# Optimization experiments

Hardware: AMD Instinct MI355X
Metric: run time of the kernel (lower is better)

Reference implementation:

```python
import jax, jax.numpy as jnp
import numpy as np

N = 10000
E = 320000
F_IN = 256
HID = 64
HEADS = 8
NUM_CLASSES = 2
NEG_SLOPE = 0.2


def _glorot(key, shape):
    fan_in, fan_out = shape[0], shape[-1]
    lim = (6.0 / (fan_in + fan_out)) ** 0.5
    return jax.random.uniform(key, shape, jnp.float32, -lim, lim)


def setup_inputs() -> dict:
    key = jax.random.key(0)
    ks = jax.random.split(key, 20)
    x = jax.random.normal(ks[0], (N, F_IN), jnp.float32)
    edge_index = jax.random.randint(ks[1], (2, E), 0, N, jnp.int64)
    d = {
        "x": x,
        "edge_index": edge_index,
        # layer 1: in=256 -> heads=8, C=64, concat -> 512
        "W1": _glorot(ks[2], (F_IN, HEADS * HID)),
        "a_src1": _glorot(ks[3], (HEADS, HID)),
        "a_dst1": _glorot(ks[4], (HEADS, HID)),
        "b1": jnp.zeros((HEADS * HID,), jnp.float32),
        # layer 2: in=512 -> heads=8, C=64, concat -> 512
        "W2": _glorot(ks[5], (HEADS * HID, HEADS * HID)),
        "a_src2": _glorot(ks[6], (HEADS, HID)),
        "a_dst2": _glorot(ks[7], (HEADS, HID)),
        "b2": jnp.zeros((HEADS * HID,), jnp.float32),
        # output conv: in=512 -> heads=1, C=64, no concat
        "W3": _glorot(ks[8], (HEADS * HID, HID)),
        "a_src3": _glorot(ks[9], (1, HID)),
        "a_dst3": _glorot(ks[10], (1, HID)),
        "b3": jnp.zeros((HID,), jnp.float32),
        # classifier
        "lin_W": _glorot(ks[11], (HID, NUM_CLASSES)),
        "lin_b": jnp.zeros((NUM_CLASSES,), jnp.float32),
    }
    return d


def _gat_layer(x, src, dst, W, a_src, a_dst, b, heads, ch, concat):
    # project: [N, H, C]
    h = (x @ W).reshape(-1, heads, ch)
    alpha_src = jnp.sum(h * a_src, axis=-1)  # [N, H]
    alpha_dst = jnp.sum(h * a_dst, axis=-1)  # [N, H]
    # per-edge attention logits (edge j -> i uses src alpha of j, dst alpha of i)
    e = jax.nn.leaky_relu(alpha_src[src] + alpha_dst[dst], NEG_SLOPE)  # [E, H]
    # segment softmax over incoming edges of each destination node
    m = jax.ops.segment_max(e, dst, num_segments=N)  # [N, H]
    m = jnp.where(jnp.isfinite(m), m, 0.0)
    ex = jnp.exp(e - m[dst])
    denom = jax.ops.segment_sum(ex, dst, num_segments=N)
    alpha = ex / (denom[dst] + 1e-16)  # [E, H]
    # weighted message aggregation
    out = jax.ops.segment_sum(h[src] * alpha[:, :, None], dst, num_segments=N)  # [N, H, C]
    if concat:
        out = out.reshape(N, heads * ch)
    else:
        out = out.mean(axis=1)
    return out + b


def reference(x, edge_index, W1, a_src1, a_dst1, b1, W2, a_src2, a_dst2, b2,
              W3, a_src3, a_dst3, b3, lin_W, lin_b):
    # PyG GATConv adds self loops by default
    loop = jnp.arange(N, dtype=edge_index.dtype)
    src = jnp.concatenate([edge_index[0], loop])
    dst = jnp.concatenate([edge_index[1], loop])

    h = _gat_layer(x, src, dst, W1, a_src1, a_dst1, b1, HEADS, HID, True)
    h = jax.nn.elu(h)
    h = _gat_layer(h, src, dst, W2, a_src2, a_dst2, b2, HEADS, HID, True)
    h = jax.nn.elu(h)
    h = _gat_layer(h, src, dst, W3, a_src3, a_dst3, b3, 1, HID, False)
    logits = h @ lin_W + lin_b
    return jax.nn.log_softmax(logits, axis=1)
```

## Files before the change

### kernel.cpp

```cpp
#include <hip/hip_runtime.h>
#include <cmath>

#define NEG 0.2f

typedef __bf16 bf16x8 __attribute__((ext_vector_type(8)));
typedef float  f32x4  __attribute__((ext_vector_type(4)));

__device__ __forceinline__ void async16(const __bf16* g, __bf16* l) {
  __builtin_amdgcn_global_load_lds(
      (const __attribute__((address_space(1))) void*)g,
      (__attribute__((address_space(3))) void*)l, 16, 0, 0);
}
__device__ __forceinline__ f32x4 mfma16(bf16x8 a, bf16x8 b, f32x4 c) {
  return __builtin_amdgcn_mfma_f32_16x16x32_bf16(a, b, c, 0, 0, 0);
}

__global__ void count_kernel(const int* __restrict__ ei, int* __restrict__ counts, int E, int Nn) {
  int e = blockIdx.x * blockDim.x + threadIdx.x;
  if (e >= E + Nn) return;
  int d = (e < E) ? ei[E + e] : (e - E);
  atomicAdd(&counts[d], 1);
}

__global__ __launch_bounds__(1024) void scan_kernel(const int* __restrict__ counts,
                                                    int* __restrict__ row_ptr,
                                                    int* __restrict__ cursor,
                                                    int n, int total) {
  __shared__ int sums[1024];
  int t = threadIdx.x;
  int per = (n + 1023) >> 10;
  int base = t * per;
  int s = 0;
  for (int i = 0; i < per; ++i) { int idx = base + i; if (idx < n) s += counts[idx]; }
  sums[t] = s;
  __syncthreads();
  for (int st = 1; st < 1024; st <<= 1) {
    int v = (t >= st) ? sums[t - st] : 0;
    __syncthreads();
    sums[t] += v;
    __syncthreads();
  }
  int off = (t == 0) ? 0 : sums[t - 1];
  for (int i = 0; i < per; ++i) {
    int idx = base + i;
    if (idx < n) { row_ptr[idx] = off; cursor[idx] = off; off += counts[idx]; }
  }
  if (t == 0) row_ptr[n] = total;
}

__global__ void scatter_kernel(const int* __restrict__ ei, int* __restrict__ cursor,
                               int* __restrict__ src_sorted, int E, int Nn) {
  int e = blockIdx.x * blockDim.x + threadIdx.x;
  if (e >= E + Nn) return;
  int s, d;
  if (e < E) { s = ei[e]; d = ei[E + e]; } else { s = e - E; d = e - E; }
  int pos = atomicAdd(&cursor[d], 1);
  src_sorted[pos] = s;
}

__global__ void prep_kernel(const float* __restrict__ x, __bf16* __restrict__ xsh,
                            __bf16* __restrict__ xsl,
                            const float* __restrict__ W1, __bf16* __restrict__ W1th,
                            const float* __restrict__ W2, __bf16* __restrict__ W2th,
                            const float* __restrict__ W3, __bf16* __restrict__ W3th,
                            int* __restrict__ counts, int Nn) {
  int i = blockIdx.x * blockDim.x + threadIdx.x;
  if (i < Nn) { counts[i] = 0; return; }
  i -= Nn;
  int nx = Nn * 256;
  if (i < nx) {
    float v = x[i];
    __bf16 h = (__bf16)v;
    xsh[i] = h;
    xsl[i] = (__bf16)(v - (float)h);
    return;
  }
  i -= nx;
  if (i < 256 * 512) {
    int k = i / 512, c = i % 512;
    W1th[(size_t)c * 256 + k] = (__bf16)W1[i];
    return;
  }
  i -= 256 * 512;
  if (i < 512 * 512) {
    int k = i / 512, c = i % 512;
    W2th[(size_t)c * 512 + k] = (__bf16)W2[i];
    return;
  }
  i -= 512 * 512;
  if (i < 512 * 64) {
    int k = i / 64, c = i % 64;
    W3th[(size_t)c * 512 + k] = (__bf16)W3[i];
    return;
  }
}

template <bool ASPLIT>
__global__ __launch_bounds__(256, 4) void gemm_v3(
    const __bf16* __restrict__ Ah, const __bf16* __restrict__ Al,
    const __bf16* __restrict__ Bth,
    __bf16* __restrict__ Cb,
    const float* __restrict__ asrc, const float* __restrict__ adst,
    float* __restrict__ als, float* __restrict__ ald,
    int M, int K, int Nc, int PX) {
  __shared__ __bf16 sAh[64 * 64], sBh[128 * 64];
  __shared__ __bf16 sAl[ASPLIT ? 64 * 64 : 64];

  int p = blockIdx.x;
  int c = p & 7, j = p >> 3;
  int x = c * PX + (j >> 2);
  int y = j & 3;
  int rowBase = x * 64, colBase = y * 128;
  if (rowBase >= M) return;

  int tid = threadIdx.x;
  int lane = tid & 63, wave = tid >> 6;
  int r16 = lane & 15, koct = lane >> 4, msk = r16 & 7;

  int fa0 = tid, fa1 = 256 + tid;
  int ar0 = fa0 >> 3, ar1 = fa1 >> 3;
  int as0 = (fa0 & 7) ^ (ar0 & 7);
  int as1 = (fa1 & 7) ^ (ar1 & 7);
  size_t aoff0 = (size_t)min(rowBase + ar0, M - 1) * K + as0 * 8;
  size_t aoff1 = (size_t)min(rowBase + ar1, M - 1) * K + as1 * 8;
  size_t boff[4];
#pragma unroll
  for (int r = 0; r < 4; ++r) {
    int f = r * 256 + tid;
    int col = f >> 3;
    int s = (f & 7) ^ (col & 7);
    boff[r] = (size_t)(colBase + col) * K + s * 8;
  }
  int lb0 = (wave * 64) * 8;
  int lb1 = ((256 + wave * 64)) * 8;
  int lb2 = ((512 + wave * 64)) * 8;
  int lb3 = ((768 + wave * 64)) * 8;

  int arow = wave * 16 + r16;
  f32x4 acc[8] = {};

  for (int k0 = 0; k0 < K; k0 += 64) {
    __syncthreads();
    async16(Ah + aoff0 + k0, sAh + lb0);
    async16(Ah + aoff1 + k0, sAh + lb1);
    if (ASPLIT) {
      async16(Al + aoff0 + k0, sAl + lb0);
      async16(Al + aoff1 + k0, sAl + lb1);
    }
    async16(Bth + boff[0] + k0, sBh + lb0);
    async16(Bth + boff[1] + k0, sBh + lb1);
    async16(Bth + boff[2] + k0, sBh + lb2);
    async16(Bth + boff[3] + k0, sBh + lb3);
    __syncthreads();

#pragma unroll
    for (int kk = 0; kk < 2; ++kk) {
      int ks = ((kk * 4 + koct) ^ msk) * 8;
      bf16x8 ah = *reinterpret_cast<const bf16x8*>(sAh + arow * 64 + ks);
      bf16x8 al;
      if (ASPLIT) al = *reinterpret_cast<const bf16x8*>(sAl + arow * 64 + ks);
      bf16x8 bh[8];
#pragma unroll
      for (int fn = 0; fn < 8; ++fn)
        bh[fn] = *reinterpret_cast<const bf16x8*>(sBh + (fn * 16 + r16) * 64 + ks);
#pragma unroll
      for (int fn = 0; fn < 8; ++fn) {
        acc[fn] = mfma16(ah, bh[fn], acc[fn]);
        if (ASPLIT) acc[fn] = mfma16(al, bh[fn], acc[fn]);
      }
    }
  }

  float asv[8], adv[8];
#pragma unroll
  for (int fn = 0; fn < 8; ++fn) {
    int ai = (y * 2 + (fn >> 2)) * 64 + (fn & 3) * 16 + r16;
    asv[fn] = asrc[ai];
    adv[fn] = adst[ai];
  }
#pragma unroll
  for (int r = 0; r < 4; ++r) {
    int row = rowBase + wave * 16 + koct * 4 + r;
    float psA = 0.f, pdA = 0.f, psB = 0.f, pdB = 0.f;
#pragma unroll
    for (int fn = 0; fn < 8; ++fn) {
      float v = acc[fn][r];
      if (row < M) Cb[(size_t)row * Nc + colBase + fn * 16 + r16] = (__bf16)v;
      if (fn < 4) { psA = fmaf(v, asv[fn], psA); pdA = fmaf(v, adv[fn], pdA); }
      else        { psB = fmaf(v, asv[fn], psB); pdB = fmaf(v, adv[fn], pdB); }
    }
#pragma unroll
    for (int sft = 1; sft < 16; sft <<= 1) {
      psA += __shfl_xor(psA, sft); pdA += __shfl_xor(pdA, sft);
      psB += __shfl_xor(psB, sft); pdB += __shfl_xor(pdB, sft);
    }
    if (r16 == 0 && row < M) {
      als[(size_t)row * 8 + y * 2 + 0] = psA;
      ald[(size_t)row * 8 + y * 2 + 0] = pdA;
      als[(size_t)row * 8 + y * 2 + 1] = psB;
      ald[(size_t)row * 8 + y * 2 + 1] = pdB;
    }
  }
}

__global__ __launch_bounds__(256, 4) void gemm_v2(
    const __bf16* __restrict__ Ah,
    const __bf16* __restrict__ Bth,
    float* __restrict__ Cf,
    const float* __restrict__ asrc, const float* __restrict__ adst,
    float* __restrict__ als, float* __restrict__ ald,
    int M, int K, int Nc) {
  __shared__ __bf16 sAh[128 * 64], sBh[64 * 64];

  int x = blockIdx.x;
  int rowBase = x * 128, colBase = 0;
  if (rowBase >= M) return;

  int tid = threadIdx.x;
  int lane = tid & 63, wave = tid >> 6;
  int r16 = lane & 15, koct = lane >> 4, msk = r16 & 7;

  f32x4 acc[2][4] = {};

  for (int k0 = 0; k0 < K; k0 += 64) {
    __syncthreads();
#pragma unroll
    for (int r = 0; r < 4; ++r) {
      int flat = r * 256 + tid;
      int row = flat >> 3;
      int grow = rowBase + row;
      if (grow >= M) grow = M - 1;
      int s = (flat & 7) ^ (row & 7);
      size_t go = (size_t)grow * K + k0 + s * 8;
      int lb = (r * 256 + wave * 64) * 8;
      async16(Ah + go, sAh + lb);
    }
#pragma unroll
    for (int r = 0; r < 2; ++r) {
      int flat = r * 256 + tid;
      int col = flat >> 3;
      int s = (flat & 7) ^ (col & 7);
      size_t go = (size_t)(colBase + col) * K + k0 + s * 8;
      int lb = (r * 256 + wave * 64) * 8;
      async16(Bth + go, sBh + lb);
    }
    __syncthreads();

#pragma unroll
    for (int kk = 0; kk < 2; ++kk) {
      bf16x8 ah[2], bh[4];
#pragma unroll
      for (int fm = 0; fm < 2; ++fm) {
        int off = (wave * 32 + fm * 16 + r16) * 64 + (((kk * 4 + koct) ^ msk) * 8);
        ah[fm] = *reinterpret_cast<const bf16x8*>(sAh + off);
      }
#pragma unroll
      for (int fn = 0; fn < 4; ++fn) {
        int off = (fn * 16 + r16) * 64 + (((kk * 4 + koct) ^ msk) * 8);
        bh[fn] = *reinterpret_cast<const bf16x8*>(sBh + off);
      }
#pragma unroll
      for (int fm = 0; fm < 2; ++fm)
#pragma unroll
        for (int fn = 0; fn < 4; ++fn)
          acc[fm][fn] = mfma16(ah[fm], bh[fn], acc[fm][fn]);
    }
  }

  float asv[4], adv[4];
#pragma unroll
  for (int fn = 0; fn < 4; ++fn) {
    asv[fn] = asrc[fn * 16 + r16];
    adv[fn] = adst[fn * 16 + r16];
  }
#pragma unroll
  for (int fm = 0; fm < 2; ++fm)
#pragma unroll
    for (int r = 0; r < 4; ++r) {
      int row = rowBase + wave * 32 + fm * 16 + koct * 4 + r;
      float ps = 0.f, pd = 0.f;
#pragma unroll
      for (int fn = 0; fn < 4; ++fn) {
        float v = acc[fm][fn][r];
        ps = fmaf(v, asv[fn], ps);
        pd = fmaf(v, adv[fn], pd);
        if (row < M) Cf[(size_t)row * Nc + fn * 16 + r16] = v;
      }
#pragma unroll
      for (int sft = 1; sft < 16; sft <<= 1) {
        ps += __shfl_xor(ps, sft);
        pd += __shfl_xor(pd, sft);
      }
      if (r16 == 0 && row < M) {
        als[row] = ps;
        ald[row] = pd;
      }
    }
}

__global__ __launch_bounds__(256) void agg8v4_kernel(const __bf16* __restrict__ Hb,
                                                     const float* __restrict__ als,
                                                     const float* __restrict__ ald,
                                                     const float* __restrict__ bias,
                                                     const int* __restrict__ row_ptr,
                                                     const int* __restrict__ src_sorted,
                                                     __bf16* __restrict__ Oh,
                                                     int Nn) {
  int c8 = blockIdx.x & 7;
  int sl = c8 >> 1;
  int chunk = (blockIdx.x >> 3) * 2 + (c8 & 1);
  int lane = threadIdx.x & 63, wave = threadIdx.x >> 6;
  int sub = lane >> 4;
  int cg = lane & 15;
  int n = chunk * 16 + wave * 4 + sub;
  bool alive = (n < Nn);
  if (!alive) n = Nn - 1;
  int head = sl * 2 + (cg >> 3);
  int colb = head * 64 + (cg & 7) * 8;

  int start = row_ptr[n], deg = row_ptr[n + 1] - start;
  float aldn = ald[n * 8 + head];
  int dm = deg;
  dm = max(dm, __shfl_xor(dm, 16));
  dm = max(dm, __shfl_xor(dm, 32));

  float acc[8] = {};
  float ssum = 0.f;
  float mrun = 0.f;
  const __bf16* hcol = Hb + colb;
  for (int e0 = 0; e0 < dm; e0 += 8) {
    int idx[8];
    float lv[8];
    bf16x8 v[8];
#pragma unroll
    for (int i = 0; i < 8; ++i) {
      int e = e0 + i;
      if (e > deg - 1) e = deg - 1;
      idx[i] = src_sorted[start + e];
    }
#pragma unroll
    for (int i = 0; i < 8; ++i) lv[i] = als[idx[i] * 8 + head];
#pragma unroll
    for (int i = 0; i < 8; ++i)
      v[i] = *reinterpret_cast<const bf16x8*>(hcol + (size_t)idx[i] * 512);
    float lm = -INFINITY;
#pragma unroll
    for (int i = 0; i < 8; ++i) {
      float l = lv[i] + aldn;
      l = l > 0.f ? l : NEG * l;
      lv[i] = l;
      lm = fmaxf(lm, l);
    }
    if (__builtin_expect(lm > mrun + 24.f, 0)) {
      float sc = __expf(mrun - lm);
      ssum *= sc;
#pragma unroll
      for (int j = 0; j < 8; ++j) acc[j] *= sc;
      mrun = lm;
    }
#pragma unroll
    for (int i = 0; i < 8; ++i) {
      float w = (e0 + i < deg) ? __expf(lv[i] - mrun) : 0.f;
      ssum += w;
#pragma unroll
      for (int j = 0; j < 8; ++j) acc[j] = fmaf(w, (float)v[i][j], acc[j]);
    }
  }

  if (alive) {
    float inv = 1.f / (ssum + 1e-16f);
    bf16x8 vh;
#pragma unroll
    for (int j = 0; j < 8; ++j) {
      float v = acc[j] * inv + bias[colb + j];
      v = v > 0.f ? v : expm1f(v);
      vh[j] = (__bf16)v;
    }
    *reinterpret_cast<bf16x8*>(Oh + (size_t)n * 512 + colb) = vh;
  }
}

__global__ __launch_bounds__(256) void agg1cls_kernel(const float* __restrict__ Hf,
                                                      const float* __restrict__ als,
                                                      const float* __restrict__ ald,
                                                      const float* __restrict__ bias,
                                                      const int* __restrict__ row_ptr,
                                                      const int* __restrict__ src_sorted,
                                                      const float* __restrict__ lw,
                                                      const float* __restrict__ lb,
                                                      float* __restrict__ out,
                                                      int Nn) {
  int n = (blockIdx.x * 256 + threadIdx.x) >> 6;
  if (n >= Nn) return;
  int lane = threadIdx.x & 63;
  int start = row_ptr[n], deg = row_ptr[n + 1] - start;
  float aldn = ald[n];

  float acc = 0.f, ssum = 0.f, mrun = 0.f;
  for (int e0 = 0; e0 < deg; e0 += 8) {
    int idx[8];
    float lv[8], hv[8];
#pragma unroll
    for (int i = 0; i < 8; ++i) {
      int e = e0 + i;
      if (e > deg - 1) e = deg - 1;
      idx[i] = src_sorted[start + e];
    }
#pragma unroll
    for (int i = 0; i < 8; ++i) lv[i] = als[idx[i]];
#pragma unroll
    for (int i = 0; i < 8; ++i) hv[i] = Hf[(size_t)idx[i] * 64 + lane];
    float lm = -INFINITY;
#pragma unroll
    for (int i = 0; i < 8; ++i) {
      float l = lv[i] + aldn;
      l = l > 0.f ? l : NEG * l;
      lv[i] = l;
      lm = fmaxf(lm, l);
    }
    if (__builtin_expect(lm > mrun + 24.f, 0)) {
      float sc = __expf(mrun - lm);
      ssum *= sc;
      acc *= sc;
      mrun = lm;
    }
#pragma unroll
    for (int i = 0; i < 8; ++i) {
      float w = (e0 + i < deg) ? __expf(lv[i] - mrun) : 0.f;
      ssum += w;
      acc = fmaf(w, hv[i], acc);
    }
  }
  float o = acc / (ssum + 1e-16f) + bias[lane];

  float p0 = o * lw[lane * 2 + 0];
  float p1 = o * lw[lane * 2 + 1];
  for (int s = 32; s; s >>= 1) {
    p0 += __shfl_xor(p0, s);
    p1 += __shfl_xor(p1, s);
  }
  if (lane == 0) {
    p0 += lb[0];
    p1 += lb[1];
    float mx = fmaxf(p0, p1);
    float lse = mx + logf(expf(p0 - mx) + expf(p1 - mx));
    out[n * 2 + 0] = p0 - lse;
    out[n * 2 + 1] = p1 - lse;
  }
}

extern "C" void kernel_launch(void* const* d_in, const int* in_sizes, int n_in,
                              void* d_out, int out_size, void* d_ws, size_t ws_size,
                              hipStream_t stream) {
  (void)n_in; (void)out_size; (void)ws_size;
  const float* x     = (const float*)d_in[0];
  const int*   ei    = (const int*)d_in[1];
  const float* W1    = (const float*)d_in[2];
  const float* asrc1 = (const float*)d_in[3];
  const float* adst1 = (const float*)d_in[4];
  const float* b1    = (const float*)d_in[5];
  const float* W2    = (const float*)d_in[6];
  const float* asrc2 = (const float*)d_in[7];
  const float* adst2 = (const float*)d_in[8];
  const float* b2    = (const float*)d_in[9];
  const float* W3    = (const float*)d_in[10];
  const float* asrc3 = (const float*)d_in[11];
  const float* adst3 = (const float*)d_in[12];
  const float* b3    = (const float*)d_in[13];
  const float* linW  = (const float*)d_in[14];
  const float* linb  = (const float*)d_in[15];
  float* out = (float*)d_out;

  int Nn = in_sizes[0] / 256;
  int E  = in_sizes[1] / 2;
  int E2 = E + Nn;

  char* w = (char*)d_ws;
  auto carve = [&](size_t bytes) {
    char* p = w;
    w += (bytes + 63) & ~(size_t)63;
    return p;
  };
  __bf16* xsh  = (__bf16*)carve((size_t)Nn * 256 * 2);
  __bf16* xsl  = (__bf16*)carve((size_t)Nn * 256 * 2);
  __bf16* Ahb  = (__bf16*)carve((size_t)Nn * 512 * 2);
  __bf16* Hb16 = (__bf16*)carve((size_t)Nn * 512 * 2);
  float*  Hb3  = (float*)carve((size_t)Nn * 64 * 4);
  float*  als  = (float*)carve((size_t)Nn * 8 * 4);
  float*  ald  = (float*)carve((size_t)Nn * 8 * 4);
  __bf16* W1th = (__bf16*)carve(256 * 512 * 2);
  __bf16* W2th = (__bf16*)carve(512 * 512 * 2);
  __bf16* W3th = (__bf16*)carve(512 * 64 * 2);
  int* counts     = (int*)carve((size_t)Nn * 4);
  int* cursor     = (int*)carve((size_t)Nn * 4);
  int* row_ptr    = (int*)carve(((size_t)Nn + 1) * 4);
  int* src_sorted = (int*)carve((size_t)E2 * 4);

  int prep_total = Nn + Nn * 256 + 256 * 512 + 512 * 512 + 512 * 64;
  prep_kernel<<<(prep_total + 255) / 256, 256, 0, stream>>>(
      x, xsh, xsl, W1, W1th, W2, W2th, W3, W3th, counts, Nn);
  count_kernel<<<(E2 + 255) / 256, 256, 0, stream>>>(ei, counts, E, Nn);
  scan_kernel<<<1, 1024, 0, stream>>>(counts, row_ptr, cursor, Nn, E2);
  scatter_kernel<<<(E2 + 255) / 256, 256, 0, stream>>>(ei, cursor, src_sorted, E, Nn);

  int gx64 = (Nn + 63) / 64;
  int PX3 = (gx64 + 7) / 8;
  int nblk3 = 8 * PX3 * 4;
  int gx128 = (Nn + 127) / 128;
  int ga = (Nn + 3) / 4;
  int gv4 = ((Nn + 31) / 32) * 8;

  gemm_v3<true><<<nblk3, 256, 0, stream>>>(xsh, xsl, W1th, Hb16,
                                           asrc1, adst1, als, ald, Nn, 256, 512, PX3);
  agg8v4_kernel<<<gv4, 256, 0, stream>>>(Hb16, als, ald, b1, row_ptr, src_sorted, Ahb, Nn);
  gemm_v3<false><<<nblk3, 256, 0, stream>>>(Ahb, nullptr, W2th, Hb16,
                                            asrc2, adst2, als, ald, Nn, 512, 512, PX3);
  agg8v4_kernel<<<gv4, 256, 0, stream>>>(Hb16, als, ald, b2, row_ptr, src_sorted, Ahb, Nn);
  gemm_v2<<<gx128, 256, 0, stream>>>(Ahb, W3th, Hb3,
                                     asrc3, adst3, als, ald, Nn, 512, 64);
  agg1cls_kernel<<<ga, 256, 0, stream>>>(Hb3, als, ald, b3, row_ptr, src_sorted,
                                         linW, linb, out, Nn);
}
```

Before: 199.0 us.

## Sort nodes by in-degree to balance per-wave work in 8-head aggregation

Adds a degree histogram, scan and scatter pass that builds a permutation of nodes grouped by in-degree (capped at 511). The two 8-head aggregation kernels then process nodes in this order, so the four nodes sharing a wave, whose loop runs to the largest degree among them, have similar degrees. The aim is to cut the wasted iterations on masked edges. The cost is three extra small kernel launches, atomics, and scattered output writes and row_ptr reads, because neighbouring threads no longer handle neighbouring node ids.

```diff
diff --git a/kernel.cpp b/kernel.cpp
--- a/kernel.cpp
+++ b/kernel.cpp
@@ -58,15 +58,50 @@
   src_sorted[pos] = s;
 }
 
+__global__ void dhist_kernel(const int* __restrict__ row_ptr, int* __restrict__ hist, int Nn) {
+  int n = blockIdx.x * blockDim.x + threadIdx.x;
+  if (n >= Nn) return;
+  int d = row_ptr[n + 1] - row_ptr[n];
+  if (d > 511) d = 511;
+  atomicAdd(&hist[d], 1);
+}
+
+__global__ __launch_bounds__(512) void dscan_kernel(const int* __restrict__ hist,
+                                                    int* __restrict__ dcur) {
+  __shared__ int s[512];
+  int t = threadIdx.x;
+  s[t] = hist[t];
+  __syncthreads();
+  for (int st = 1; st < 512; st <<= 1) {
+    int v = (t >= st) ? s[t - st] : 0;
+    __syncthreads();
+    s[t] += v;
+    __syncthreads();
+  }
+  dcur[t] = (t == 0) ? 0 : s[t - 1];
+}
+
+__global__ void dscatter_kernel(const int* __restrict__ row_ptr, int* __restrict__ dcur,
+                                int* __restrict__ perm, int Nn) {
+  int n = blockIdx.x * blockDim.x + threadIdx.x;
+  if (n >= Nn) return;
+  int d = row_ptr[n + 1] - row_ptr[n];
+  if (d > 511) d = 511;
+  int pos = atomicAdd(&dcur[d], 1);
+  perm[pos] = n;
+}
+
 __global__ void prep_kernel(const float* __restrict__ x, __bf16* __restrict__ xsh,
                             __bf16* __restrict__ xsl,
                             const float* __restrict__ W1, __bf16* __restrict__ W1th,
                             const float* __restrict__ W2, __bf16* __restrict__ W2th,
                             const float* __restrict__ W3, __bf16* __restrict__ W3th,
-                            int* __restrict__ counts, int Nn) {
+                            int* __restrict__ counts, int* __restrict__ hist, int Nn) {
   int i = blockIdx.x * blockDim.x + threadIdx.x;
   if (i < Nn) { counts[i] = 0; return; }
   i -= Nn;
+  if (i < 512) { hist[i] = 0; return; }
+  i -= 512;
   int nx = Nn * 256;
   if (i < nx) {
     float v = x[i];
@@ -304,6 +339,7 @@
                                                      const float* __restrict__ bias,
                                                      const int* __restrict__ row_ptr,
                                                      const int* __restrict__ src_sorted,
+                                                     const int* __restrict__ perm,
                                                      __bf16* __restrict__ Oh,
                                                      int Nn) {
   int c8 = blockIdx.x & 7;
@@ -312,9 +348,9 @@
   int lane = threadIdx.x & 63, wave = threadIdx.x >> 6;
   int sub = lane >> 4;
   int cg = lane & 15;
-  int n = chunk * 16 + wave * 4 + sub;
-  bool alive = (n < Nn);
-  if (!alive) n = Nn - 1;
+  int i = chunk * 16 + wave * 4 + sub;
+  bool alive = (i < Nn);
+  int n = perm[alive ? i : Nn - 1];
   int head = sl * 2 + (cg >> 3);
   int colb = head * 64 + (cg & 7) * 8;
 
@@ -333,22 +369,22 @@
     float lv[8];
     bf16x8 v[8];
 #pragma unroll
-    for (int i = 0; i < 8; ++i) {
-      int e = e0 + i;
+    for (int i2 = 0; i2 < 8; ++i2) {
+      int e = e0 + i2;
       if (e > deg - 1) e = deg - 1;
-      idx[i] = src_sorted[start + e];
-    }
-#pragma unroll
-    for (int i = 0; i < 8; ++i) lv[i] = als[idx[i] * 8 + head];
-#pragma unroll
-    for (int i = 0; i < 8; ++i)
-      v[i] = *reinterpret_cast<const bf16x8*>(hcol + (size_t)idx[i] * 512);
+      idx[i2] = src_sorted[start + e];
+    }
+#pragma unroll
+    for (int i2 = 0; i2 < 8; ++i2) lv[i2] = als[idx[i2] * 8 + head];
+#pragma unroll
+    for (int i2 = 0; i2 < 8; ++i2)
+      v[i2] = *reinterpret_cast<const bf16x8*>(hcol + (size_t)idx[i2] * 512);
     float lm = -INFINITY;
 #pragma unroll
-    for (int i = 0; i < 8; ++i) {
-      float l = lv[i] + aldn;
+    for (int i2 = 0; i2 < 8; ++i2) {
+      float l = lv[i2] + aldn;
       l = l > 0.f ? l : NEG * l;
-      lv[i] = l;
+      lv[i2] = l;
       lm = fmaxf(lm, l);
     }
     if (__builtin_expect(lm > mrun + 24.f, 0)) {
@@ -359,11 +395,11 @@
       mrun = lm;
     }
 #pragma unroll
-    for (int i = 0; i < 8; ++i) {
-      float w = (e0 + i < deg) ? __expf(lv[i] - mrun) : 0.f;
+    for (int i2 = 0; i2 < 8; ++i2) {
+      float w = (e0 + i2 < deg) ? __expf(lv[i2] - mrun) : 0.f;
       ssum += w;
 #pragma unroll
-      for (int j = 0; j < 8; ++j) acc[j] = fmaf(w, (float)v[i][j], acc[j]);
+      for (int j = 0; j < 8; ++j) acc[j] = fmaf(w, (float)v[i2][j], acc[j]);
     }
   }
 
@@ -495,13 +531,19 @@
   int* cursor     = (int*)carve((size_t)Nn * 4);
   int* row_ptr    = (int*)carve(((size_t)Nn + 1) * 4);
   int* src_sorted = (int*)carve((size_t)E2 * 4);
-
-  int prep_total = Nn + Nn * 256 + 256 * 512 + 512 * 512 + 512 * 64;
+  int* hist       = (int*)carve(512 * 4);
+  int* dcur       = (int*)carve(512 * 4);
+  int* perm       = (int*)carve((size_t)Nn * 4);
+
+  int prep_total = Nn + 512 + Nn * 256 + 256 * 512 + 512 * 512 + 512 * 64;
   prep_kernel<<<(prep_total + 255) / 256, 256, 0, stream>>>(
-      x, xsh, xsl, W1, W1th, W2, W2th, W3, W3th, counts, Nn);
+      x, xsh, xsl, W1, W1th, W2, W2th, W3, W3th, counts, hist, Nn);
   count_kernel<<<(E2 + 255) / 256, 256, 0, stream>>>(ei, counts, E, Nn);
   scan_kernel<<<1, 1024, 0, stream>>>(counts, row_ptr, cursor, Nn, E2);
   scatter_kernel<<<(E2 + 255) / 256, 256, 0, stream>>>(ei, cursor, src_sorted, E, Nn);
+  dhist_kernel<<<(Nn + 255) / 256, 256, 0, stream>>>(row_ptr, hist, Nn);
+  dscan_kernel<<<1, 512, 0, stream>>>(hist, dcur);
+  dscatter_kernel<<<(Nn + 255) / 256, 256, 0, stream>>>(row_ptr, dcur, perm, Nn);
 
   int gx64 = (Nn + 63) / 64;
   int PX3 = (gx64 + 7) / 8;
@@ -512,10 +554,10 @@
 
   gemm_v3<true><<<nblk3, 256, 0, stream>>>(xsh, xsl, W1th, Hb16,
                                            asrc1, adst1, als, ald, Nn, 256, 512, PX3);
-  agg8v4_kernel<<<gv4, 256, 0, stream>>>(Hb16, als, ald, b1, row_ptr, src_sorted, Ahb, Nn);
+  agg8v4_kernel<<<gv4, 256, 0, stream>>>(Hb16, als, ald, b1, row_ptr, src_sorted, perm, Ahb, Nn);
   gemm_v3<false><<<nblk3, 256, 0, stream>>>(Ahb, nullptr, W2th, Hb16,
                                             asrc2, adst2, als, ald, Nn, 512, 512, PX3);
-  agg8v4_kernel<<<gv4, 256, 0, stream>>>(Hb16, als, ald, b2, row_ptr, src_sorted, Ahb, Nn);
+  agg8v4_kernel<<<gv4, 256, 0, stream>>>(Hb16, als, ald, b2, row_ptr, src_sorted, perm, Ahb, Nn);
   gemm_v2<<<gx128, 256, 0, stream>>>(Ahb, W3th, Hb3,
                                      asrc3, adst3, als, ald, Nn, 512, 64);
   agg1cls_kernel<<<ga, 256, 0, stream>>>(Hb3, als, ald, b3, row_ptr, src_sorted,
```

Measured after the change: 248.9 us. 1.25x slower.
